# Performance work log

Measured on AMD Instinct MI355X. Metric: run time of the kernel, lower is better.

## Reference

```python
import jax, jax.numpy as jnp
import numpy as np

EPS = 1e-06
FLOW_SCALE = 8.0  # pixels of typical displacement


def setup_inputs() -> dict:
    key = jax.random.key(0)
    k1, k2, k3 = jax.random.split(key, 3)
    N, H, W = 8, 720, 1280
    img = jax.random.uniform(k1, (N, 1, H, W), dtype=jnp.float32)
    counts = jax.random.uniform(k2, (N, 1, H, W), dtype=jnp.float32)
    flo = jax.random.normal(k3, (N, 2, H, W), dtype=jnp.float32) * FLOW_SCALE
    return {"img": img, "counts": counts, "flo": flo}


def _sample_one(img, counts, sx, sy, w):
    """Splat img*counts*w and counts*w to integer-shifted locations (scatter-add).
    sx, sy: integer-valued float shifts along H and W axes, shape (N,C,H,W)."""
    N, C, H, W = img.shape
    bx = jnp.arange(H, dtype=jnp.int32)[:, None]            # (H,1) row index
    by = jnp.arange(W, dtype=jnp.int32)[None, :]            # (1,W) col index
    ix = sx.astype(jnp.int32) + bx                          # (N,C,H,W) target row
    iy = sy.astype(jnp.int32) + by                          # (N,C,H,W) target col
    mask = (ix >= 0) & (ix < H) & (iy >= 0) & (iy < W)
    bn = jnp.arange(N, dtype=jnp.int32)[:, None, None, None]
    bc = jnp.arange(C, dtype=jnp.int32)[None, :, None, None]
    ids = ((bn * C + bc) * H + jnp.clip(ix, 0, H - 1)) * W + jnp.clip(iy, 0, W - 1)
    cw = counts * w
    val = jnp.where(mask, img * cw, 0.0).reshape(-1)
    one = jnp.where(mask, cw, 0.0).reshape(-1)
    flat_ids = ids.reshape(-1)
    size = N * C * H * W
    img_warp = jnp.zeros((size,), dtype=img.dtype).at[flat_ids].add(val)
    one_warp = jnp.zeros((size,), dtype=img.dtype).at[flat_ids].add(one)
    return img_warp.reshape(N, C, H, W), one_warp.reshape(N, C, H, W)


def reference(img, counts, flo):
    N, C, H, W = img.shape
    y = flo[:, 0:1]                    # shift along H axis
    x = flo[:, 1:2]                    # shift along W axis? NOTE: original maps x->H-shift
    # Original code: x = flo[:,1:2] used as shiftx (row), y = flo[:,0:1] as shifty (col)
    x = jnp.broadcast_to(x, (N, C, H, W))
    y = jnp.broadcast_to(y, (N, C, H, W))
    x1 = jnp.floor(x)
    x2 = x1 + 1.0
    y1 = jnp.floor(y)
    y2 = y1 + 1.0
    # normalized gaussian corner weights
    dx1 = (x - x1) ** 2
    dx2 = (x - x2) ** 2
    dy1 = (y - y1) ** 2
    dy2 = (y - y2) ** 2
    w11 = jnp.exp(-(dx1 + dy1))
    w12 = jnp.exp(-(dx1 + dy2))
    w21 = jnp.exp(-(dx2 + dy1))
    w22 = jnp.exp(-(dx2 + dy2))
    s = w11 + w12 + w21 + w22
    w11, w12, w21, w22 = w11 / s, w12 / s, w21 / s, w22 / s
    i11, o11 = _sample_one(img, counts, x1, y1, w11)
    i12, o12 = _sample_one(img, counts, x1, y2, w12)
    i21, o21 = _sample_one(img, counts, x2, y1, w21)
    i22, o22 = _sample_one(img, counts, x2, y2, w22)
    imgw = i11 + i12 + i21 + i22
    o = o11 + o12 + o21 + o22
    return imgw / (o + EPS), o
```

## Files before the change

### kernel.cpp

```cpp
#include <hip/hip_runtime.h>

#define EPS 1e-6f

constexpr int N_ = 8;
constexpr int H_ = 720;
constexpr int W_ = 1280;
constexpr int HW = H_ * W_;
constexpr int NPIX = N_ * HW;

constexpr int TH = 120;
constexpr int TW = 80;
constexpr int R_ = 16;
constexpr int LH = TH + 2 * R_;
constexpr int LW = TW + 2 * R_;
constexpr int LSZ = LH * LW;
constexpr int TILES_H = H_ / TH;
constexpr int TILES_W = W_ / TW;
constexpr int TILES_PER_IMG = TILES_H * TILES_W;
constexpr size_t WS_PER_IMG = (size_t)TILES_PER_IMG * LSZ * 2 * sizeof(float);

#define QSCALE 67108864.0f
#define QINV   (1.0f / 67108864.0f)

__device__ __forceinline__ void atomic_fadd(float* p, float v) {
    unsafeAtomicAdd(p, v);
}

__global__ __launch_bounds__(512) void splat_tiled_kernel(
        const float* __restrict__ img,
        const float* __restrict__ counts,
        const float* __restrict__ flo,
        float* __restrict__ ws,
        float* __restrict__ fb_img,
        float* __restrict__ fb_one,
        int n0) {
    __shared__ __align__(16) unsigned long long s_acc[LSZ];

    int bt = blockIdx.x;
    int tc = bt % TILES_W;
    int t2 = bt / TILES_W;
    int tr = t2 % TILES_H;
    int n  = n0 + t2 / TILES_H;
    int row0 = tr * TH;
    int col0 = tc * TW;
    int tid = threadIdx.x;

    {
        float4 z = make_float4(0.f, 0.f, 0.f, 0.f);
        float4* z0 = (float4*)s_acc;
        for (int i = tid; i < LSZ / 2; i += 512) z0[i] = z;
    }
    __syncthreads();

    int nbase = n * HW;
    int fbase_n = n * 2 * HW;

    for (int p = tid; p < TH * TW; p += 512) {
        int r = p / TW;
        int c = p % TW;
        int h = row0 + r;
        int w = col0 + c;
        int idx = nbase + h * W_ + w;

        float iv = img[idx];
        float cv = counts[idx];
        int fo = fbase_n + h * W_ + w;
        float y = flo[fo];
        float x = flo[fo + HW];

        float x1 = floorf(x);
        float y1 = floorf(y);
        float fx = x - x1;
        float fy = y - y1;
        float gx = 1.0f - fx;
        float gy = 1.0f - fy;
        float ex1 = __expf(-fx * fx);
        float ex2 = __expf(-gx * gx);
        float ey1 = __expf(-fy * fy);
        float ey2 = __expf(-gy * gy);

        float s = (ex1 + ex2) * (ey1 + ey2);
        float inv = cv / s;

        int ix1 = (int)x1 + h;
        int iy1 = (int)y1 + w;

        int ixr[2] = {ix1, ix1 + 1};
        int iyc[2] = {iy1, iy1 + 1};
        float wx[2] = {ex1, ex2};
        float wy[2] = {ey1, ey2};

        #pragma unroll
        for (int a = 0; a < 2; ++a) {
            #pragma unroll
            for (int b = 0; b < 2; ++b) {
                float ww = wx[a] * wy[b] * inv;
                float wi = iv * ww;
                int lh = ixr[a] - row0 + R_;
                int lw = iyc[b] - col0 + R_;
                if ((unsigned)lh < (unsigned)LH && (unsigned)lw < (unsigned)LW) {
                    int o = lh * LW + lw;
                    unsigned qi = (unsigned)(wi * QSCALE + 0.5f);
                    unsigned qw = (unsigned)(ww * QSCALE + 0.5f);
                    atomicAdd(&s_acc[o],
                              ((unsigned long long)qi << 32) |
                               (unsigned long long)qw);
                } else if ((unsigned)ixr[a] < (unsigned)H_ &&
                           (unsigned)iyc[b] < (unsigned)W_) {
                    int o = nbase + ixr[a] * W_ + iyc[b];
                    atomic_fadd(fb_img + o, wi);
                    atomic_fadd(fb_one + o, ww);
                }
            }
        }
    }
    __syncthreads();

    float2* wsb = (float2*)(ws + (size_t)bt * LSZ * 2);
    for (int i = tid; i < LSZ; i += 512) {
        unsigned long long v = s_acc[i];
        float2 o2;
        o2.x = (float)(unsigned)(v >> 32) * QINV;
        o2.y = (float)(unsigned)(v & 0xffffffffu) * QINV;
        wsb[i] = o2;
    }
}

__global__ __launch_bounds__(256) void gather_kernel(
        const float* __restrict__ ws,
        float* __restrict__ out0,
        float* __restrict__ out1,
        int n0, int npix_chunk) {
    int pidx = (blockIdx.x * 256 + threadIdx.x) * 4;
    if (pidx >= npix_chunk) return;
    int w0 = pidx % W_;
    int t = pidx / W_;
    int h = t % H_;
    int nl = t / H_;

    int gidx = (n0 + nl) * HW + h * W_ + w0;

    float4 fi = *(const float4*)(out0 + gidx);
    float4 fo = *(const float4*)(out1 + gidx);

    int tr_lo = (h >= R_) ? (h - R_) / TH : 0;
    int tr_hi = (h + R_) / TH; if (tr_hi > TILES_H - 1) tr_hi = TILES_H - 1;
    int tc_lo = (w0 >= R_) ? (w0 - R_) / TW : 0;
    int tc_hi = (w0 + 3 + R_) / TW; if (tc_hi > TILES_W - 1) tc_hi = TILES_W - 1;

    for (int tr = tr_lo; tr <= tr_hi; ++tr) {
        int lh = h - tr * TH + R_;
        for (int tc = tc_lo; tc <= tc_hi; ++tc) {
            int lw0 = w0 - tc * TW + R_;
            const float* bp = ws
                + ((size_t)((nl * TILES_H + tr) * TILES_W + tc)) * (LSZ * 2)
                + (size_t)(lh * LW + lw0) * 2;
            float4 a = *(const float4*)bp;
            float4 b = *(const float4*)(bp + 4);
            fi.x += a.x; fo.x += a.y;
            fi.y += a.z; fo.y += a.w;
            fi.z += b.x; fo.z += b.y;
            fi.w += b.z; fo.w += b.w;
        }
    }
    float4 r;
    r.x = fi.x / (fo.x + EPS);
    r.y = fi.y / (fo.y + EPS);
    r.z = fi.z / (fo.z + EPS);
    r.w = fi.w / (fo.w + EPS);
    *(float4*)(out0 + gidx) = r;
    *(float4*)(out1 + gidx) = fo;
}

__global__ void splat_atomic_kernel(const float* __restrict__ img,
                                    const float* __restrict__ counts,
                                    const float* __restrict__ flo,
                                    float* __restrict__ acc_img,
                                    float* __restrict__ acc_one) {
    int idx = blockIdx.x * blockDim.x + threadIdx.x;
    if (idx >= NPIX) return;
    int w = idx % W_;
    int t = idx / W_;
    int h = t % H_;
    int n = t / H_;

    float iv = img[idx];
    float cv = counts[idx];
    int fbase = ((n * 2) * H_ + h) * W_ + w;
    float y = flo[fbase];
    float x = flo[fbase + HW];

    float x1 = floorf(x);
    float y1 = floorf(y);
    float fx = x - x1, fy = y - y1;
    float gx = 1.0f - fx, gy = 1.0f - fy;
    float ex1 = __expf(-fx * fx), ex2 = __expf(-gx * gx);
    float ey1 = __expf(-fy * fy), ey2 = __expf(-gy * gy);
    float s = (ex1 + ex2) * (ey1 + ey2);
    float inv = cv / s;

    int ix1 = (int)x1 + h, ix2 = ix1 + 1;
    int iy1 = (int)y1 + w, iy2 = iy1 + 1;
    int nbase = n * HW;
    if ((unsigned)ix1 < (unsigned)H_ && (unsigned)iy1 < (unsigned)W_) {
        int o = nbase + ix1 * W_ + iy1; float ww = ex1 * ey1 * inv;
        atomic_fadd(acc_img + o, iv * ww); atomic_fadd(acc_one + o, ww);
    }
    if ((unsigned)ix1 < (unsigned)H_ && (unsigned)iy2 < (unsigned)W_) {
        int o = nbase + ix1 * W_ + iy2; float ww = ex1 * ey2 * inv;
        atomic_fadd(acc_img + o, iv * ww); atomic_fadd(acc_one + o, ww);
    }
    if ((unsigned)ix2 < (unsigned)H_ && (unsigned)iy1 < (unsigned)W_) {
        int o = nbase + ix2 * W_ + iy1; float ww = ex2 * ey1 * inv;
        atomic_fadd(acc_img + o, iv * ww); atomic_fadd(acc_one + o, ww);
    }
    if ((unsigned)ix2 < (unsigned)H_ && (unsigned)iy2 < (unsigned)W_) {
        int o = nbase + ix2 * W_ + iy2; float ww = ex2 * ey2 * inv;
        atomic_fadd(acc_img + o, iv * ww); atomic_fadd(acc_one + o, ww);
    }
}

__global__ void finalize_kernel(float* __restrict__ out0,
                                const float* __restrict__ out1) {
    int idx = blockIdx.x * blockDim.x + threadIdx.x;
    if (idx >= NPIX) return;
    out0[idx] = out0[idx] / (out1[idx] + EPS);
}

extern "C" void kernel_launch(void* const* d_in, const int* in_sizes, int n_in,
                              void* d_out, int out_size, void* d_ws, size_t ws_size,
                              hipStream_t stream) {
    const float* img    = (const float*)d_in[0];
    const float* counts = (const float*)d_in[1];
    const float* flo    = (const float*)d_in[2];

    float* out0 = (float*)d_out;
    float* out1 = out0 + NPIX;

    hipMemsetAsync(d_out, 0, (size_t)2 * NPIX * sizeof(float), stream);

    int ipc = (int)(ws_size / WS_PER_IMG);
    if (ipc > N_) ipc = N_;

    if (ipc >= 1) {
        float* ws = (float*)d_ws;
        for (int n0 = 0; n0 < N_; n0 += ipc) {
            int ni = (n0 + ipc <= N_) ? ipc : (N_ - n0);
            splat_tiled_kernel<<<ni * TILES_PER_IMG, 512, 0, stream>>>(
                img, counts, flo, ws, out0, out1, n0);
            int npix_chunk = ni * HW;
            gather_kernel<<<(npix_chunk / 4 + 255) / 256, 256, 0, stream>>>(
                ws, out0, out1, n0, npix_chunk);
        }
    } else {
        const int threads = 256;
        const int blocks = (NPIX + threads - 1) / threads;
        splat_atomic_kernel<<<blocks, threads, 0, stream>>>(img, counts, flo,
                                                            out0, out1);
        finalize_kernel<<<blocks, threads, 0, stream>>>(out0, out1);
    }
}
```

Baseline: 238.9 us.

## Flush tile accumulators via packed 64-bit global atomics instead of workspace gather

The splat kernel now writes its shared-memory tile results straight into a global packed 64-bit fixed-point accumulator with atomicAdd, skipping zero entries. This replaces the per-tile workspace write and the multi-tile gather kernel. Out-of-halo fallback splats use the same packed atomics, so only one atomic is issued per corner instead of two float atomics. The finalize step becomes a simple streaming unpack-and-divide. The cost is global 64-bit atomics on halo overlaps and a memset of a buffer twice the size of one output plane.

```diff
diff --git a/kernel.cpp b/kernel.cpp
--- a/kernel.cpp
+++ b/kernel.cpp
@@ -17,7 +17,6 @@
 constexpr int TILES_H = H_ / TH;
 constexpr int TILES_W = W_ / TW;
 constexpr int TILES_PER_IMG = TILES_H * TILES_W;
-constexpr size_t WS_PER_IMG = (size_t)TILES_PER_IMG * LSZ * 2 * sizeof(float);
 
 #define QSCALE 67108864.0f
 #define QINV   (1.0f / 67108864.0f)
@@ -30,17 +29,14 @@
         const float* __restrict__ img,
         const float* __restrict__ counts,
         const float* __restrict__ flo,
-        float* __restrict__ ws,
-        float* __restrict__ fb_img,
-        float* __restrict__ fb_one,
-        int n0) {
+        unsigned long long* __restrict__ acc) {
     __shared__ __align__(16) unsigned long long s_acc[LSZ];
 
     int bt = blockIdx.x;
     int tc = bt % TILES_W;
     int t2 = bt / TILES_W;
     int tr = t2 % TILES_H;
-    int n  = n0 + t2 / TILES_H;
+    int n  = t2 / TILES_H;
     int row0 = tr * TH;
     int col0 = tc * TW;
     int tid = threadIdx.x;
@@ -96,80 +92,63 @@
             for (int b = 0; b < 2; ++b) {
                 float ww = wx[a] * wy[b] * inv;
                 float wi = iv * ww;
+                unsigned qi = (unsigned)(wi * QSCALE + 0.5f);
+                unsigned qw = (unsigned)(ww * QSCALE + 0.5f);
+                unsigned long long pk =
+                    ((unsigned long long)qi << 32) | (unsigned long long)qw;
                 int lh = ixr[a] - row0 + R_;
                 int lw = iyc[b] - col0 + R_;
                 if ((unsigned)lh < (unsigned)LH && (unsigned)lw < (unsigned)LW) {
-                    int o = lh * LW + lw;
-                    unsigned qi = (unsigned)(wi * QSCALE + 0.5f);
-                    unsigned qw = (unsigned)(ww * QSCALE + 0.5f);
-                    atomicAdd(&s_acc[o],
-                              ((unsigned long long)qi << 32) |
-                               (unsigned long long)qw);
+                    atomicAdd(&s_acc[lh * LW + lw], pk);
                 } else if ((unsigned)ixr[a] < (unsigned)H_ &&
                            (unsigned)iyc[b] < (unsigned)W_) {
-                    int o = nbase + ixr[a] * W_ + iyc[b];
-                    atomic_fadd(fb_img + o, wi);
-                    atomic_fadd(fb_one + o, ww);
+                    atomicAdd(&acc[nbase + ixr[a] * W_ + iyc[b]], pk);
                 }
             }
         }
     }
     __syncthreads();
 
-    float2* wsb = (float2*)(ws + (size_t)bt * LSZ * 2);
     for (int i = tid; i < LSZ; i += 512) {
         unsigned long long v = s_acc[i];
-        float2 o2;
-        o2.x = (float)(unsigned)(v >> 32) * QINV;
-        o2.y = (float)(unsigned)(v & 0xffffffffu) * QINV;
-        wsb[i] = o2;
-    }
-}
-
-__global__ __launch_bounds__(256) void gather_kernel(
-        const float* __restrict__ ws,
+        if (v == 0ull) continue;
+        int lh = i / LW;
+        int lw = i - lh * LW;
+        int gr = row0 - R_ + lh;
+        int gc = col0 - R_ + lw;
+        if ((unsigned)gr < (unsigned)H_ && (unsigned)gc < (unsigned)W_)
+            atomicAdd(&acc[nbase + gr * W_ + gc], v);
+    }
+}
+
+__global__ __launch_bounds__(256) void finalize_packed_kernel(
+        const unsigned long long* __restrict__ acc,
         float* __restrict__ out0,
-        float* __restrict__ out1,
-        int n0, int npix_chunk) {
-    int pidx = (blockIdx.x * 256 + threadIdx.x) * 4;
-    if (pidx >= npix_chunk) return;
-    int w0 = pidx % W_;
-    int t = pidx / W_;
-    int h = t % H_;
-    int nl = t / H_;
-
-    int gidx = (n0 + nl) * HW + h * W_ + w0;
-
-    float4 fi = *(const float4*)(out0 + gidx);
-    float4 fo = *(const float4*)(out1 + gidx);
-
-    int tr_lo = (h >= R_) ? (h - R_) / TH : 0;
-    int tr_hi = (h + R_) / TH; if (tr_hi > TILES_H - 1) tr_hi = TILES_H - 1;
-    int tc_lo = (w0 >= R_) ? (w0 - R_) / TW : 0;
-    int tc_hi = (w0 + 3 + R_) / TW; if (tc_hi > TILES_W - 1) tc_hi = TILES_W - 1;
-
-    for (int tr = tr_lo; tr <= tr_hi; ++tr) {
-        int lh = h - tr * TH + R_;
-        for (int tc = tc_lo; tc <= tc_hi; ++tc) {
-            int lw0 = w0 - tc * TW + R_;
-            const float* bp = ws
-                + ((size_t)((nl * TILES_H + tr) * TILES_W + tc)) * (LSZ * 2)
-                + (size_t)(lh * LW + lw0) * 2;
-            float4 a = *(const float4*)bp;
-            float4 b = *(const float4*)(bp + 4);
-            fi.x += a.x; fo.x += a.y;
-            fi.y += a.z; fo.y += a.w;
-            fi.z += b.x; fo.z += b.y;
-            fi.w += b.z; fo.w += b.w;
-        }
-    }
+        float* __restrict__ out1) {
+    int i4 = (blockIdx.x * 256 + threadIdx.x) * 4;
+    if (i4 >= NPIX) return;
+
+    const ulonglong2* a2 = (const ulonglong2*)(acc + i4);
+    ulonglong2 p0 = a2[0];
+    ulonglong2 p1 = a2[1];
+
+    float4 fi, fo;
+    fi.x = (float)(unsigned)(p0.x >> 32) * QINV;
+    fo.x = (float)(unsigned)(p0.x & 0xffffffffull) * QINV;
+    fi.y = (float)(unsigned)(p0.y >> 32) * QINV;
+    fo.y = (float)(unsigned)(p0.y & 0xffffffffull) * QINV;
+    fi.z = (float)(unsigned)(p1.x >> 32) * QINV;
+    fo.z = (float)(unsigned)(p1.x & 0xffffffffull) * QINV;
+    fi.w = (float)(unsigned)(p1.y >> 32) * QINV;
+    fo.w = (float)(unsigned)(p1.y & 0xffffffffull) * QINV;
+
     float4 r;
     r.x = fi.x / (fo.x + EPS);
     r.y = fi.y / (fo.y + EPS);
     r.z = fi.z / (fo.z + EPS);
     r.w = fi.w / (fo.w + EPS);
-    *(float4*)(out0 + gidx) = r;
-    *(float4*)(out1 + gidx) = fo;
+    *(float4*)(out0 + i4) = r;
+    *(float4*)(out1 + i4) = fo;
 }
 
 __global__ void splat_atomic_kernel(const float* __restrict__ img,
@@ -237,22 +216,16 @@
     float* out0 = (float*)d_out;
     float* out1 = out0 + NPIX;
 
-    hipMemsetAsync(d_out, 0, (size_t)2 * NPIX * sizeof(float), stream);
-
-    int ipc = (int)(ws_size / WS_PER_IMG);
-    if (ipc > N_) ipc = N_;
-
-    if (ipc >= 1) {
-        float* ws = (float*)d_ws;
-        for (int n0 = 0; n0 < N_; n0 += ipc) {
-            int ni = (n0 + ipc <= N_) ? ipc : (N_ - n0);
-            splat_tiled_kernel<<<ni * TILES_PER_IMG, 512, 0, stream>>>(
-                img, counts, flo, ws, out0, out1, n0);
-            int npix_chunk = ni * HW;
-            gather_kernel<<<(npix_chunk / 4 + 255) / 256, 256, 0, stream>>>(
-                ws, out0, out1, n0, npix_chunk);
-        }
+    if (ws_size >= (size_t)NPIX * sizeof(unsigned long long)) {
+        unsigned long long* acc = (unsigned long long*)d_ws;
+        hipMemsetAsync(acc, 0, (size_t)NPIX * sizeof(unsigned long long),
+                       stream);
+        splat_tiled_kernel<<<N_ * TILES_PER_IMG, 512, 0, stream>>>(
+            img, counts, flo, acc);
+        finalize_packed_kernel<<<NPIX / 4 / 256, 256, 0, stream>>>(
+            acc, out0, out1);
     } else {
+        hipMemsetAsync(d_out, 0, (size_t)2 * NPIX * sizeof(float), stream);
         const int threads = 256;
         const int blocks = (NPIX + threads - 1) / threads;
         splat_atomic_kernel<<<blocks, threads, 0, stream>>>(img, counts, flo,
```

Result: slower. 260.1 us (+8.9%).
